# Kernel optimization log

Measured on AMD Instinct MI355X. Metric: run time of the kernel, lower is better.

The kernel has to match this reference:

```python
import jax, jax.numpy as jnp
import numpy as np

N = 10000
E = 320000
IN, HID, OUT = 512, 128, 128
HEADS, GC = 4, 64
NEG_SLOPE = 0.2


def setup_inputs() -> dict:
    key = jax.random.key(0)
    ks = jax.random.split(key, 12)
    inp = {
        'x': jax.random.normal(ks[0], (N, IN), dtype=jnp.float32),
        'edge_index': jax.random.randint(ks[1], (2, E), 0, N, dtype=jnp.int64),
        # encoder params
        'W1': jax.random.normal(ks[2], (IN, HID), dtype=jnp.float32) / np.sqrt(IN),
        'b1': jnp.zeros((HID,), dtype=jnp.float32),
        'W2': jax.random.normal(ks[3], (HID, OUT), dtype=jnp.float32) / np.sqrt(HID),
        'b2': jnp.zeros((OUT,), dtype=jnp.float32),
        # GATConv params: lin weight [OUT, HEADS*GC], att vectors [HEADS, GC], bias [HEADS*GC]
        'Wg': jax.random.normal(ks[4], (OUT, HEADS * GC), dtype=jnp.float32) / np.sqrt(OUT),
        'att_src': jax.random.normal(ks[5], (HEADS, GC), dtype=jnp.float32) * 0.1,
        'att_dst': jax.random.normal(ks[6], (HEADS, GC), dtype=jnp.float32) * 0.1,
        'bias_g': jnp.zeros((HEADS * GC,), dtype=jnp.float32),
    }
    return inp


def _forward(x, W1, b1, W2, b2, Wg, att_src, att_dst, bias_g, edge_index):
    # encoder: Linear -> ReLU -> Linear
    h = jax.nn.relu(x @ W1 + b1) @ W2 + b2  # [N, OUT]
    # GATConv adds self-loops by default
    loops = jnp.arange(N, dtype=edge_index.dtype)
    src = jnp.concatenate([edge_index[0], loops])  # message sources j
    dst = jnp.concatenate([edge_index[1], loops])  # message targets i
    # per-head linear transform
    g = (h @ Wg).reshape(N, HEADS, GC)  # [N, H, C]
    a_src = jnp.sum(g * att_src, axis=-1)  # [N, H]
    a_dst = jnp.sum(g * att_dst, axis=-1)  # [N, H]
    e = a_src[src] + a_dst[dst]            # [E+N, H]
    e = jax.nn.leaky_relu(e, NEG_SLOPE)
    # segment softmax over incoming edges of each destination node
    m = jax.ops.segment_max(e, dst, num_segments=N)  # [N, H]
    ex = jnp.exp(e - m[dst])
    s = jax.ops.segment_sum(ex, dst, num_segments=N)  # [N, H]
    alpha = ex / s[dst]                    # [E+N, H]
    # weighted scatter-aggregate of source features
    out = jax.ops.segment_sum(g[src] * alpha[:, :, None], dst, num_segments=N)  # [N, H, C]
    return out.reshape(N, HEADS * GC) + bias_g


def reference(x, edge_index, W1, b1, W2, b2, Wg, att_src, att_dst, bias_g):
    return _forward(x, W1, b1, W2, b2, Wg, att_src, att_dst, bias_g, edge_index)
```

## Files before the change

kernel.cpp:

```cpp
#include <hip/hip_runtime.h>

#define N_NODES 10000
#define N_EDGES 320000
#define DIM_IN  512
#define DIM_HID 128
#define HC      256
#define NEG_SLOPE 0.2f
#define SLOT    96

typedef short short8 __attribute__((ext_vector_type(8)));
typedef float floatx4 __attribute__((ext_vector_type(4)));

__device__ __forceinline__ unsigned short f2bf(float x) {
  unsigned int u = __float_as_uint(x);
  u += 0x7FFFu + ((u >> 16) & 1u);
  return (unsigned short)(u >> 16);
}

__global__ __launch_bounds__(256) void prep_kernel(
    const float* __restrict__ W2, const float* __restrict__ Wg,
    const float* __restrict__ b2, const float* __restrict__ W1,
    const float* __restrict__ x,
    unsigned short* __restrict__ WfT, float* __restrict__ bfuse,
    unsigned short* __restrict__ W1T, unsigned short* __restrict__ xb,
    int* __restrict__ cursor) {
  __shared__ float Ast[16][68];
  __shared__ float Bsf[16][64];
  __shared__ unsigned short td[32][33];
  const int t = threadIdx.x;
  const int b = blockIdx.x;
  if (b >= 76) {
    const int base = (b - 76) * 2048 + t * 8;
    const float4 v0 = *(const float4*)(x + base);
    const float4 v1 = *(const float4*)(x + base + 4);
    ushort4 s0 = {f2bf(v0.x), f2bf(v0.y), f2bf(v0.z), f2bf(v0.w)};
    ushort4 s1 = {f2bf(v1.x), f2bf(v1.y), f2bf(v1.z), f2bf(v1.w)};
    *(ushort4*)(xb + base)     = s0;
    *(ushort4*)(xb + base + 4) = s1;
    return;
  }
  if (b < 12) {
    const int flat = b * 256 + t;
    if (flat < (N_NODES + 3) / 4) ((int4*)cursor)[flat] = make_int4(0, 0, 0, 0);
    const int bx = b >> 2, by = b & 3;
    const int tx = t & 15, ty = t >> 4;
    const int m0 = bx * 64, n0 = by * 64;
    const int ar = t >> 2, ac4 = (t & 3) * 4;
    const int br = t >> 4, bc4 = (t & 15) * 4;
    const int arow = m0 + ar;
    float acc[4][4] = {};
    float4 av, bv, avn, bvn;
    auto gload = [&](int k0, float4& a4, float4& b4) {
      if (arow < DIM_HID)       a4 = *(const float4*)(W2 + (size_t)arow * DIM_HID + k0 + ac4);
      else if (arow == DIM_HID) a4 = *(const float4*)(b2 + k0 + ac4);
      else                      a4 = make_float4(0.f, 0.f, 0.f, 0.f);
      b4 = *(const float4*)(Wg + (size_t)(k0 + br) * HC + n0 + bc4);
    };
    gload(0, av, bv);
    for (int k0 = 0; k0 < DIM_HID; k0 += 16) {
      Ast[ac4 + 0][ar] = av.x; Ast[ac4 + 1][ar] = av.y;
      Ast[ac4 + 2][ar] = av.z; Ast[ac4 + 3][ar] = av.w;
      *(float4*)&Bsf[br][bc4] = bv;
      __syncthreads();
      if (k0 + 16 < DIM_HID) gload(k0 + 16, avn, bvn);
#pragma unroll
      for (int kk = 0; kk < 16; ++kk) {
        const float4 a = *(const float4*)&Ast[kk][ty * 4];
        const float4 bq = *(const float4*)&Bsf[kk][tx * 4];
        const float as[4] = {a.x, a.y, a.z, a.w};
        const float bs[4] = {bq.x, bq.y, bq.z, bq.w};
#pragma unroll
        for (int i = 0; i < 4; ++i)
#pragma unroll
          for (int j = 0; j < 4; ++j) acc[i][j] = fmaf(as[i], bs[j], acc[i][j]);
      }
      __syncthreads();
      av = avn; bv = bvn;
    }
#pragma unroll
    for (int i = 0; i < 4; ++i) {
      const int row = m0 + ty * 4 + i;
#pragma unroll
      for (int j = 0; j < 4; ++j) {
        const int col = n0 + tx * 4 + j;
        if (row < DIM_HID)       WfT[(size_t)col * DIM_HID + row] = f2bf(acc[i][j]);
        else if (row == DIM_HID) bfuse[col] = acc[i][j];
      }
    }
  } else {
    const int bb = b - 12;
    const int r0 = (bb >> 2) * 32, c0 = (bb & 3) * 32;
    const int tx = t & 31, ty = t >> 5;
#pragma unroll
    for (int p = 0; p < 4; ++p)
      td[tx][ty + p * 8] = f2bf(W1[(size_t)(r0 + ty + p * 8) * DIM_HID + c0 + tx]);
    __syncthreads();
#pragma unroll
    for (int p = 0; p < 4; ++p)
      W1T[(size_t)(c0 + ty + p * 8) * DIM_IN + r0 + tx] = td[ty + p * 8][tx];
  }
}

__global__ __launch_bounds__(256) void gemm1_kernel(
    const unsigned short* __restrict__ xb, const unsigned short* __restrict__ W1T,
    const float* __restrict__ b1, unsigned short* __restrict__ h1b) {
  constexpr int K = DIM_IN, N = DIM_HID, BK = 32;
  __shared__ unsigned short As[64][48];
  __shared__ unsigned short Bs[32][48];
  const int t = threadIdx.x;
  const int m0 = blockIdx.x * 64, n0 = blockIdx.y * 32;
  const int w = t >> 6, L = t & 63, lm = L & 15, q = L >> 4;
  floatx4 acc[2] = {};
  uint4 ab, abn;
  uint2 bb, bbn;
  auto ld = [&](int kb, uint4& va, uint2& vb) {
    va = *(const uint4*)(xb + (size_t)(m0 + (t >> 2)) * K + kb + (t & 3) * 8);
    vb = *(const uint2*)(W1T + (size_t)(n0 + (t >> 3)) * K + kb + (t & 7) * 4);
  };
  constexpr int NT = K / BK;
  ld(0, ab, bb);
  for (int kt = 0; kt < NT; ++kt) {
    *(uint4*)&As[t >> 2][(t & 3) * 8] = ab;
    *(uint2*)&Bs[t >> 3][(t & 7) * 4] = bb;
    __syncthreads();
    if (kt + 1 < NT) ld((kt + 1) * BK, abn, bbn);
    const short8 af = *(const short8*)&As[w * 16 + lm][q * 8];
#pragma unroll
    for (int nt = 0; nt < 2; ++nt) {
      const short8 bf = *(const short8*)&Bs[nt * 16 + lm][q * 8];
      acc[nt] = __builtin_amdgcn_mfma_f32_16x16x32_bf16(af, bf, acc[nt], 0, 0, 0);
    }
    __syncthreads();
    ab = abn; bb = bbn;
  }
  const int row0 = m0 + w * 16 + q * 4;
#pragma unroll
  for (int nt = 0; nt < 2; ++nt) {
    const int col = n0 + nt * 16 + lm;
    const float bv = b1[col];
#pragma unroll
    for (int r = 0; r < 4; ++r)
      if (row0 + r < N_NODES)
        h1b[(size_t)(row0 + r) * N + col] = f2bf(fmaxf(acc[nt][r] + bv, 0.f));
  }
}

__global__ __launch_bounds__(256) void gemm2_kernel(
    const unsigned short* __restrict__ h1b, const unsigned short* __restrict__ WfT,
    const float* __restrict__ bfuse, unsigned short* __restrict__ g,
    const float* __restrict__ att_src, const float* __restrict__ att_dst,
    float* __restrict__ a_src, float* __restrict__ a_dst,
    const int* __restrict__ e_src, const int* __restrict__ e_dst,
    int* __restrict__ cursor, int* __restrict__ src_sorted) {
  constexpr int K = DIM_HID, N = HC, BK = 32;
  __shared__ unsigned short As[64][48];
  __shared__ unsigned short Bs[64][48];
  const int t = threadIdx.x;
  {
    const int nthr = gridDim.x * gridDim.y * 256;
    const int flat = (blockIdx.y * gridDim.x + blockIdx.x) * 256 + t;
    for (int id = flat; id < N_EDGES + N_NODES; id += nthr) {
      int s, d;
      if (id < N_EDGES) { s = e_src[id]; d = e_dst[id]; }
      else              { s = d = id - N_EDGES; }
      src_sorted[d * SLOT + atomicAdd(&cursor[d], 1)] = s;
    }
  }
  const int m0 = blockIdx.x * 64, n0 = blockIdx.y * 64;
  const int w = t >> 6, L = t & 63, lm = L & 15, q = L >> 4;
  floatx4 acc[4] = {};
  uint4 ab, abn, bb, bbn;
  auto ld = [&](int kb, uint4& va, uint4& vb) {
    va = *(const uint4*)(h1b + (size_t)(m0 + (t >> 2)) * K + kb + (t & 3) * 8);
    vb = *(const uint4*)(WfT + (size_t)(n0 + (t >> 2)) * K + kb + (t & 3) * 8);
  };
  constexpr int NT = K / BK;
  ld(0, ab, bb);
  for (int kt = 0; kt < NT; ++kt) {
    *(uint4*)&As[t >> 2][(t & 3) * 8] = ab;
    *(uint4*)&Bs[t >> 2][(t & 3) * 8] = bb;
    __syncthreads();
    if (kt + 1 < NT) ld((kt + 1) * BK, abn, bbn);
    const short8 af = *(const short8*)&As[w * 16 + lm][q * 8];
#pragma unroll
    for (int nt = 0; nt < 4; ++nt) {
      const short8 bf = *(const short8*)&Bs[nt * 16 + lm][q * 8];
      acc[nt] = __builtin_amdgcn_mfma_f32_16x16x32_bf16(af, bf, acc[nt], 0, 0, 0);
    }
    __syncthreads();
    ab = abn; bb = bbn;
  }
  const int row0 = m0 + w * 16 + q * 4;
  const int hh = n0 >> 6;
  float ps[4] = {}, pd[4] = {};
#pragma unroll
  for (int nt = 0; nt < 4; ++nt) {
    const int col = n0 + nt * 16 + lm;
    const float bv = bfuse[col];
    const float as_c = att_src[hh * 64 + nt * 16 + lm];
    const float ad_c = att_dst[hh * 64 + nt * 16 + lm];
#pragma unroll
    for (int r = 0; r < 4; ++r) {
      const float gv = acc[nt][r] + bv;
      if (row0 + r < N_NODES) g[(size_t)(row0 + r) * N + col] = f2bf(gv);
      ps[r] = fmaf(gv, as_c, ps[r]);
      pd[r] = fmaf(gv, ad_c, pd[r]);
    }
  }
#pragma unroll
  for (int r = 0; r < 4; ++r) {
#pragma unroll
    for (int off = 1; off < 16; off <<= 1) {
      ps[r] += __shfl_xor(ps[r], off);
      pd[r] += __shfl_xor(pd[r], off);
    }
    if (lm == 0 && row0 + r < N_NODES) {
      a_src[(row0 + r) * 4 + hh] = ps[r];
      a_dst[(row0 + r) * 4 + hh] = pd[r];
    }
  }
}

__global__ __launch_bounds__(256) void aggregate_kernel(
    const unsigned short* __restrict__ g, const float* __restrict__ a_src,
    const float* __restrict__ a_dst, const int* __restrict__ cursor,
    const int* __restrict__ src_sorted, const float* __restrict__ bias_g,
    float* __restrict__ out) {
  const int wv   = threadIdx.x >> 6;
  const int lane = threadIdx.x & 63;
  const int node = blockIdx.x * 4 + wv;
  if (node >= N_NODES) return;
  const int e2 = lane >> 5;
  const int c8 = lane & 31;
  const int h  = c8 >> 3;
  const int start = node * SLOT;
  const int end   = start + cursor[node];
  const float4 ad = *(const float4*)(a_dst + node * 4);

  float a[8] = {};
  float s_loc = 0.f;
  for (int base = start; base < end; base += 64) {
    const int rem = min(64, end - base);
    int   sidxL = 0;
    float w0 = 0.f, w1 = 0.f, w2 = 0.f, w3 = 0.f;
    if (lane < rem) {
      sidxL = src_sorted[base + lane];
      const float4 as4 = *(const float4*)(a_src + sidxL * 4);
      float e0 = as4.x + ad.x; e0 = (e0 > 0.f) ? e0 : NEG_SLOPE * e0;
      float e1 = as4.y + ad.y; e1 = (e1 > 0.f) ? e1 : NEG_SLOPE * e1;
      float ee = as4.z + ad.z; ee = (ee > 0.f) ? ee : NEG_SLOPE * ee;
      float e3 = as4.w + ad.w; e3 = (e3 > 0.f) ? e3 : NEG_SLOPE * e3;
      w0 = __expf(e0); w1 = __expf(e1); w2 = __expf(ee); w3 = __expf(e3);
    }
    const int half = (rem + 1) >> 1;
#pragma unroll 4
    for (int k = 0; k < half; ++k) {
      const int j  = 2 * k + e2;
      const int js = (j < rem) ? j : (rem - 1);
      const int sj = __shfl(sidxL, js);
      const float f0 = __shfl(w0, js), f1 = __shfl(w1, js);
      const float f2 = __shfl(w2, js), f3 = __shfl(w3, js);
      float w = (h & 2) ? ((h & 1) ? f3 : f2) : ((h & 1) ? f1 : f0);
      if (j >= rem) w = 0.f;
      const uint4 gv = *(const uint4*)(g + (size_t)sj * HC + c8 * 8);
      s_loc += w;
      a[0] = fmaf(w, __uint_as_float(gv.x << 16), a[0]);
      a[1] = fmaf(w, __uint_as_float(gv.x & 0xFFFF0000u), a[1]);
      a[2] = fmaf(w, __uint_as_float(gv.y << 16), a[2]);
      a[3] = fmaf(w, __uint_as_float(gv.y & 0xFFFF0000u), a[3]);
      a[4] = fmaf(w, __uint_as_float(gv.z << 16), a[4]);
      a[5] = fmaf(w, __uint_as_float(gv.z & 0xFFFF0000u), a[5]);
      a[6] = fmaf(w, __uint_as_float(gv.w << 16), a[6]);
      a[7] = fmaf(w, __uint_as_float(gv.w & 0xFFFF0000u), a[7]);
    }
  }
#pragma unroll
  for (int k = 0; k < 8; ++k) a[k] += __shfl_xor(a[k], 32);
  s_loc += __shfl_xor(s_loc, 32);
  if (e2 == 0) {
    const float inv = 1.f / s_loc;
    const float4 b0 = *(const float4*)(bias_g + c8 * 8);
    const float4 b1v = *(const float4*)(bias_g + c8 * 8 + 4);
    float4 o0, o1;
    o0.x = a[0] * inv + b0.x;  o0.y = a[1] * inv + b0.y;
    o0.z = a[2] * inv + b0.z;  o0.w = a[3] * inv + b0.w;
    o1.x = a[4] * inv + b1v.x; o1.y = a[5] * inv + b1v.y;
    o1.z = a[6] * inv + b1v.z; o1.w = a[7] * inv + b1v.w;
    float* op = out + (size_t)node * HC + c8 * 8;
    *(float4*)op = o0;
    *(float4*)(op + 4) = o1;
  }
}

extern "C" void kernel_launch(void* const* d_in, const int* in_sizes, int n_in,
                              void* d_out, int out_size, void* d_ws, size_t ws_size,
                              hipStream_t stream) {
  const float* x       = (const float*)d_in[0];
  const int*   ei      = (const int*)d_in[1];
  const float* W1      = (const float*)d_in[2];
  const float* b1      = (const float*)d_in[3];
  const float* W2      = (const float*)d_in[4];
  const float* b2      = (const float*)d_in[5];
  const float* Wg      = (const float*)d_in[6];
  const float* att_src = (const float*)d_in[7];
  const float* att_dst = (const float*)d_in[8];
  const float* bias_g  = (const float*)d_in[9];
  float* out = (float*)d_out;

  char* ws = (char*)d_ws;
  unsigned short* xb  = (unsigned short*)ws; ws += (size_t)(N_NODES + 64) * DIM_IN * 2;
  unsigned short* h1b = (unsigned short*)ws; ws += (size_t)(N_NODES + 64) * DIM_HID * 2;
  unsigned short* g   = (unsigned short*)ws; ws += (size_t)N_NODES * HC * 2;
  unsigned short* W1T = (unsigned short*)ws; ws += (size_t)DIM_HID * DIM_IN * 2;
  unsigned short* WfT = (unsigned short*)ws; ws += (size_t)HC * DIM_HID * 2;
  float* bfuse   = (float*)ws; ws += (size_t)HC * 4;
  float* a_src   = (float*)ws; ws += (size_t)N_NODES * 4 * 4;
  float* a_dst   = (float*)ws; ws += (size_t)N_NODES * 4 * 4;
  int* cursor    = (int*)ws;   ws += (size_t)N_NODES * 4;
  int* src_sorted= (int*)ws;   ws += (size_t)N_NODES * SLOT * 4;

  const dim3 blk(256);
  prep_kernel<<<76 + 2500, blk, 0, stream>>>(
      W2, Wg, b2, W1, x, WfT, bfuse, W1T, xb, cursor);
  gemm1_kernel<<<dim3(157, 4), blk, 0, stream>>>(xb, W1T, b1, h1b);
  gemm2_kernel<<<dim3(157, 4), blk, 0, stream>>>(
      h1b, WfT, bfuse, g, att_src, att_dst, a_src, a_dst,
      ei, ei + N_EDGES, cursor, src_sorted);
  aggregate_kernel<<<(N_NODES + 3) / 4, blk, 0, stream>>>(
      g, a_src, a_dst, cursor, src_sorted, bias_g, out);
}
```

Before: 152.2 us.

## Fuse x bf16 conversion into gemm1 and retile both GEMMs to full-width tiles

Drops the separate pass that converts x to bf16 and instead loads fp32 x directly in gemm1, converting it while staging into shared memory. That removes one write and one re-read of a 10 MB intermediate. Both GEMMs now use 32-row tiles that span the full output width, so each block reads its A rows only once, at the cost of each block staging the whole weight matrix. gemm2 maps one wave to each head for the attention dot products, and the aggregate inner loop unroll is raised from 4 to 8. The grids are smaller, so fewer blocks share the edge-bucketing work.

```diff
diff --git a/kernel.cpp b/kernel.cpp
--- a/kernel.cpp
+++ b/kernel.cpp
@@ -20,25 +20,13 @@
 __global__ __launch_bounds__(256) void prep_kernel(
     const float* __restrict__ W2, const float* __restrict__ Wg,
     const float* __restrict__ b2, const float* __restrict__ W1,
-    const float* __restrict__ x,
     unsigned short* __restrict__ WfT, float* __restrict__ bfuse,
-    unsigned short* __restrict__ W1T, unsigned short* __restrict__ xb,
-    int* __restrict__ cursor) {
+    unsigned short* __restrict__ W1T, int* __restrict__ cursor) {
   __shared__ float Ast[16][68];
   __shared__ float Bsf[16][64];
   __shared__ unsigned short td[32][33];
   const int t = threadIdx.x;
   const int b = blockIdx.x;
-  if (b >= 76) {
-    const int base = (b - 76) * 2048 + t * 8;
-    const float4 v0 = *(const float4*)(x + base);
-    const float4 v1 = *(const float4*)(x + base + 4);
-    ushort4 s0 = {f2bf(v0.x), f2bf(v0.y), f2bf(v0.z), f2bf(v0.w)};
-    ushort4 s1 = {f2bf(v1.x), f2bf(v1.y), f2bf(v1.z), f2bf(v1.w)};
-    *(ushort4*)(xb + base)     = s0;
-    *(ushort4*)(xb + base + 4) = s1;
-    return;
-  }
   if (b < 12) {
     const int flat = b * 256 + t;
     if (flat < (N_NODES + 3) / 4) ((int4*)cursor)[flat] = make_int4(0, 0, 0, 0);
@@ -102,46 +90,58 @@
 }
 
 __global__ __launch_bounds__(256) void gemm1_kernel(
-    const unsigned short* __restrict__ xb, const unsigned short* __restrict__ W1T,
+    const float* __restrict__ x, const unsigned short* __restrict__ W1T,
     const float* __restrict__ b1, unsigned short* __restrict__ h1b) {
   constexpr int K = DIM_IN, N = DIM_HID, BK = 32;
-  __shared__ unsigned short As[64][48];
-  __shared__ unsigned short Bs[32][48];
+  __shared__ unsigned short As[32][40];
+  __shared__ unsigned short Bs[128][40];
   const int t = threadIdx.x;
-  const int m0 = blockIdx.x * 64, n0 = blockIdx.y * 32;
+  const int m0 = blockIdx.x * 32;
   const int w = t >> 6, L = t & 63, lm = L & 15, q = L >> 4;
-  floatx4 acc[2] = {};
-  uint4 ab, abn;
-  uint2 bb, bbn;
-  auto ld = [&](int kb, uint4& va, uint2& vb) {
-    va = *(const uint4*)(xb + (size_t)(m0 + (t >> 2)) * K + kb + (t & 3) * 8);
-    vb = *(const uint2*)(W1T + (size_t)(n0 + (t >> 3)) * K + kb + (t & 7) * 4);
+  floatx4 acc[2][2] = {};
+  const int arow = t >> 3, akoff = (t & 7) * 4;
+  const int bcol = t >> 1, bkoff = (t & 1) * 16;
+  float4 av, avn;
+  uint4 vb0, vb1, vb0n, vb1n;
+  auto ld = [&](int kb, float4& a4, uint4& b0, uint4& b1r) {
+    a4 = (m0 + arow < N_NODES)
+        ? *(const float4*)(x + (size_t)(m0 + arow) * K + kb + akoff)
+        : make_float4(0.f, 0.f, 0.f, 0.f);
+    b0  = *(const uint4*)(W1T + (size_t)bcol * K + kb + bkoff);
+    b1r = *(const uint4*)(W1T + (size_t)bcol * K + kb + bkoff + 8);
   };
   constexpr int NT = K / BK;
-  ld(0, ab, bb);
+  ld(0, av, vb0, vb1);
   for (int kt = 0; kt < NT; ++kt) {
-    *(uint4*)&As[t >> 2][(t & 3) * 8] = ab;
-    *(uint2*)&Bs[t >> 3][(t & 7) * 4] = bb;
-    __syncthreads();
-    if (kt + 1 < NT) ld((kt + 1) * BK, abn, bbn);
-    const short8 af = *(const short8*)&As[w * 16 + lm][q * 8];
+    ushort4 s0 = {f2bf(av.x), f2bf(av.y), f2bf(av.z), f2bf(av.w)};
+    *(ushort4*)&As[arow][akoff] = s0;
+    *(uint4*)&Bs[bcol][bkoff]     = vb0;
+    *(uint4*)&Bs[bcol][bkoff + 8] = vb1;
+    __syncthreads();
+    if (kt + 1 < NT) ld((kt + 1) * BK, avn, vb0n, vb1n);
+    const short8 af0 = *(const short8*)&As[lm][q * 8];
+    const short8 af1 = *(const short8*)&As[16 + lm][q * 8];
 #pragma unroll
     for (int nt = 0; nt < 2; ++nt) {
-      const short8 bf = *(const short8*)&Bs[nt * 16 + lm][q * 8];
-      acc[nt] = __builtin_amdgcn_mfma_f32_16x16x32_bf16(af, bf, acc[nt], 0, 0, 0);
-    }
-    __syncthreads();
-    ab = abn; bb = bbn;
-  }
-  const int row0 = m0 + w * 16 + q * 4;
-#pragma unroll
-  for (int nt = 0; nt < 2; ++nt) {
-    const int col = n0 + nt * 16 + lm;
-    const float bv = b1[col];
-#pragma unroll
-    for (int r = 0; r < 4; ++r)
-      if (row0 + r < N_NODES)
-        h1b[(size_t)(row0 + r) * N + col] = f2bf(fmaxf(acc[nt][r] + bv, 0.f));
+      const short8 bf = *(const short8*)&Bs[w * 32 + nt * 16 + lm][q * 8];
+      acc[0][nt] = __builtin_amdgcn_mfma_f32_16x16x32_bf16(af0, bf, acc[0][nt], 0, 0, 0);
+      acc[1][nt] = __builtin_amdgcn_mfma_f32_16x16x32_bf16(af1, bf, acc[1][nt], 0, 0, 0);
+    }
+    __syncthreads();
+    av = avn; vb0 = vb0n; vb1 = vb1n;
+  }
+#pragma unroll
+  for (int mt = 0; mt < 2; ++mt) {
+    const int row0 = m0 + mt * 16 + q * 4;
+#pragma unroll
+    for (int nt = 0; nt < 2; ++nt) {
+      const int col = w * 32 + nt * 16 + lm;
+      const float bv = b1[col];
+#pragma unroll
+      for (int r = 0; r < 4; ++r)
+        if (row0 + r < N_NODES)
+          h1b[(size_t)(row0 + r) * N + col] = f2bf(fmaxf(acc[mt][nt][r] + bv, 0.f));
+    }
   }
 }
 
@@ -153,12 +153,12 @@
     const int* __restrict__ e_src, const int* __restrict__ e_dst,
     int* __restrict__ cursor, int* __restrict__ src_sorted) {
   constexpr int K = DIM_HID, N = HC, BK = 32;
-  __shared__ unsigned short As[64][48];
-  __shared__ unsigned short Bs[64][48];
+  __shared__ unsigned short As[32][40];
+  __shared__ unsigned short Bs[256][40];
   const int t = threadIdx.x;
   {
-    const int nthr = gridDim.x * gridDim.y * 256;
-    const int flat = (blockIdx.y * gridDim.x + blockIdx.x) * 256 + t;
+    const int nthr = gridDim.x * 256;
+    const int flat = blockIdx.x * 256 + t;
     for (int id = flat; id < N_EDGES + N_NODES; id += nthr) {
       int s, d;
       if (id < N_EDGES) { s = e_src[id]; d = e_dst[id]; }
@@ -166,57 +166,72 @@
       src_sorted[d * SLOT + atomicAdd(&cursor[d], 1)] = s;
     }
   }
-  const int m0 = blockIdx.x * 64, n0 = blockIdx.y * 64;
+  const int m0 = blockIdx.x * 32;
   const int w = t >> 6, L = t & 63, lm = L & 15, q = L >> 4;
-  floatx4 acc[4] = {};
-  uint4 ab, abn, bb, bbn;
-  auto ld = [&](int kb, uint4& va, uint4& vb) {
-    va = *(const uint4*)(h1b + (size_t)(m0 + (t >> 2)) * K + kb + (t & 3) * 8);
-    vb = *(const uint4*)(WfT + (size_t)(n0 + (t >> 2)) * K + kb + (t & 3) * 8);
+  floatx4 acc[2][4] = {};
+  const int arow = t >> 3, akoff = (t & 7) * 4;
+  uint2 va, van;
+  uint4 vb[4], vbn[4];
+  auto ld = [&](int kb, uint2& a2, uint4* b4) {
+    a2 = *(const uint2*)(h1b + (size_t)(m0 + arow) * K + kb + akoff);
+#pragma unroll
+    for (int j = 0; j < 4; ++j)
+      b4[j] = *(const uint4*)(WfT + (size_t)t * K + kb + j * 8);
   };
   constexpr int NT = K / BK;
-  ld(0, ab, bb);
+  ld(0, va, vb);
   for (int kt = 0; kt < NT; ++kt) {
-    *(uint4*)&As[t >> 2][(t & 3) * 8] = ab;
-    *(uint4*)&Bs[t >> 2][(t & 3) * 8] = bb;
-    __syncthreads();
-    if (kt + 1 < NT) ld((kt + 1) * BK, abn, bbn);
-    const short8 af = *(const short8*)&As[w * 16 + lm][q * 8];
+    *(uint2*)&As[arow][akoff] = va;
+#pragma unroll
+    for (int j = 0; j < 4; ++j) *(uint4*)&Bs[t][j * 8] = vb[j];
+    __syncthreads();
+    if (kt + 1 < NT) ld((kt + 1) * BK, van, vbn);
+    const short8 af0 = *(const short8*)&As[lm][q * 8];
+    const short8 af1 = *(const short8*)&As[16 + lm][q * 8];
 #pragma unroll
     for (int nt = 0; nt < 4; ++nt) {
-      const short8 bf = *(const short8*)&Bs[nt * 16 + lm][q * 8];
-      acc[nt] = __builtin_amdgcn_mfma_f32_16x16x32_bf16(af, bf, acc[nt], 0, 0, 0);
-    }
-    __syncthreads();
-    ab = abn; bb = bbn;
-  }
-  const int row0 = m0 + w * 16 + q * 4;
-  const int hh = n0 >> 6;
-  float ps[4] = {}, pd[4] = {};
+      const short8 bf = *(const short8*)&Bs[w * 64 + nt * 16 + lm][q * 8];
+      acc[0][nt] = __builtin_amdgcn_mfma_f32_16x16x32_bf16(af0, bf, acc[0][nt], 0, 0, 0);
+      acc[1][nt] = __builtin_amdgcn_mfma_f32_16x16x32_bf16(af1, bf, acc[1][nt], 0, 0, 0);
+    }
+    __syncthreads();
+    va = van;
+#pragma unroll
+    for (int j = 0; j < 4; ++j) vb[j] = vbn[j];
+  }
+  float ps[2][4] = {}, pd[2][4] = {};
 #pragma unroll
   for (int nt = 0; nt < 4; ++nt) {
-    const int col = n0 + nt * 16 + lm;
+    const int col = w * 64 + nt * 16 + lm;
     const float bv = bfuse[col];
-    const float as_c = att_src[hh * 64 + nt * 16 + lm];
-    const float ad_c = att_dst[hh * 64 + nt * 16 + lm];
+    const float as_c = att_src[col];
+    const float ad_c = att_dst[col];
+#pragma unroll
+    for (int mt = 0; mt < 2; ++mt) {
+      const int row0 = m0 + mt * 16 + q * 4;
+#pragma unroll
+      for (int r = 0; r < 4; ++r) {
+        const float gv = acc[mt][nt][r] + bv;
+        if (row0 + r < N_NODES) g[(size_t)(row0 + r) * N + col] = f2bf(gv);
+        ps[mt][r] = fmaf(gv, as_c, ps[mt][r]);
+        pd[mt][r] = fmaf(gv, ad_c, pd[mt][r]);
+      }
+    }
+  }
+#pragma unroll
+  for (int mt = 0; mt < 2; ++mt) {
+    const int row0 = m0 + mt * 16 + q * 4;
 #pragma unroll
     for (int r = 0; r < 4; ++r) {
-      const float gv = acc[nt][r] + bv;
-      if (row0 + r < N_NODES) g[(size_t)(row0 + r) * N + col] = f2bf(gv);
-      ps[r] = fmaf(gv, as_c, ps[r]);
-      pd[r] = fmaf(gv, ad_c, pd[r]);
-    }
-  }
-#pragma unroll
-  for (int r = 0; r < 4; ++r) {
-#pragma unroll
-    for (int off = 1; off < 16; off <<= 1) {
-      ps[r] += __shfl_xor(ps[r], off);
-      pd[r] += __shfl_xor(pd[r], off);
-    }
-    if (lm == 0 && row0 + r < N_NODES) {
-      a_src[(row0 + r) * 4 + hh] = ps[r];
-      a_dst[(row0 + r) * 4 + hh] = pd[r];
+#pragma unroll
+      for (int off = 1; off < 16; off <<= 1) {
+        ps[mt][r] += __shfl_xor(ps[mt][r], off);
+        pd[mt][r] += __shfl_xor(pd[mt][r], off);
+      }
+      if (lm == 0 && row0 + r < N_NODES) {
+        a_src[(row0 + r) * 4 + w] = ps[mt][r];
+        a_dst[(row0 + r) * 4 + w] = pd[mt][r];
+      }
     }
   }
 }
@@ -253,7 +268,7 @@
       w0 = __expf(e0); w1 = __expf(e1); w2 = __expf(ee); w3 = __expf(e3);
     }
     const int half = (rem + 1) >> 1;
-#pragma unroll 4
+#pragma unroll 8
     for (int k = 0; k < half; ++k) {
       const int j  = 2 * k + e2;
       const int js = (j < rem) ? j : (rem - 1);
@@ -308,7 +323,6 @@
   float* out = (float*)d_out;
 
   char* ws = (char*)d_ws;
-  unsigned short* xb  = (unsigned short*)ws; ws += (size_t)(N_NODES + 64) * DIM_IN * 2;
   unsigned short* h1b = (unsigned short*)ws; ws += (size_t)(N_NODES + 64) * DIM_HID * 2;
   unsigned short* g   = (unsigned short*)ws; ws += (size_t)N_NODES * HC * 2;
   unsigned short* W1T = (unsigned short*)ws; ws += (size_t)DIM_HID * DIM_IN * 2;
@@ -320,10 +334,9 @@
   int* src_sorted= (int*)ws;   ws += (size_t)N_NODES * SLOT * 4;
 
   const dim3 blk(256);
-  prep_kernel<<<76 + 2500, blk, 0, stream>>>(
-      W2, Wg, b2, W1, x, WfT, bfuse, W1T, xb, cursor);
-  gemm1_kernel<<<dim3(157, 4), blk, 0, stream>>>(xb, W1T, b1, h1b);
-  gemm2_kernel<<<dim3(157, 4), blk, 0, stream>>>(
+  prep_kernel<<<76, blk, 0, stream>>>(W2, Wg, b2, W1, WfT, bfuse, W1T, cursor);
+  gemm1_kernel<<<313, blk, 0, stream>>>(x, W1T, b1, h1b);
+  gemm2_kernel<<<313, blk, 0, stream>>>(
       h1b, WfT, bfuse, g, att_src, att_dst, a_src, a_dst,
       ei, ei + N_EDGES, cursor, src_sorted);
   aggregate_kernel<<<(N_NODES + 3) / 4, blk, 0, stream>>>(
```

Measured after the change: 167.4 us. 10.0% more time.

## Fuse x/W1 bf16 conversion into first GEMM and merge prep with it

Applied to the files above, without the earlier changes.

Removes the separate prep pass that converted x to bf16 and transposed W1. The first GEMM now loads fp32 x and W1 directly, converts them to bf16 in registers and transposes W1 into shared memory. The W2·Wg fusion and cursor zeroing run as extra blocks in the same launch. This saves one kernel launch and the round trip of the bf16 copy of x through global memory. In exchange, each of the four column blocks re-reads fp32 x at twice the bytes, and shared-memory stores for the transposed W1 tile may hit bank conflicts.

```diff
diff --git a/kernel.cpp b/kernel.cpp
--- a/kernel.cpp
+++ b/kernel.cpp
@@ -17,131 +17,122 @@
   return (unsigned short)(u >> 16);
 }
 
-__global__ __launch_bounds__(256) void prep_kernel(
+union Sm1 {
+  struct { unsigned short As[64][48]; unsigned short Bs[32][48]; } g;
+  struct { float Ast[16][68]; float Bsf[16][64]; } p;
+};
+
+__global__ __launch_bounds__(256) void fused1_kernel(
+    const float* __restrict__ x, const float* __restrict__ W1,
+    const float* __restrict__ b1,
     const float* __restrict__ W2, const float* __restrict__ Wg,
-    const float* __restrict__ b2, const float* __restrict__ W1,
-    const float* __restrict__ x,
-    unsigned short* __restrict__ WfT, float* __restrict__ bfuse,
-    unsigned short* __restrict__ W1T, unsigned short* __restrict__ xb,
-    int* __restrict__ cursor) {
-  __shared__ float Ast[16][68];
-  __shared__ float Bsf[16][64];
-  __shared__ unsigned short td[32][33];
+    const float* __restrict__ b2,
+    unsigned short* __restrict__ h1b, unsigned short* __restrict__ WfT,
+    float* __restrict__ bfuse, int* __restrict__ cursor) {
+  __shared__ Sm1 sm;
   const int t = threadIdx.x;
   const int b = blockIdx.x;
-  if (b >= 76) {
-    const int base = (b - 76) * 2048 + t * 8;
-    const float4 v0 = *(const float4*)(x + base);
-    const float4 v1 = *(const float4*)(x + base + 4);
-    ushort4 s0 = {f2bf(v0.x), f2bf(v0.y), f2bf(v0.z), f2bf(v0.w)};
-    ushort4 s1 = {f2bf(v1.x), f2bf(v1.y), f2bf(v1.z), f2bf(v1.w)};
-    *(ushort4*)(xb + base)     = s0;
-    *(ushort4*)(xb + base + 4) = s1;
-    return;
-  }
-  if (b < 12) {
-    const int flat = b * 256 + t;
-    if (flat < (N_NODES + 3) / 4) ((int4*)cursor)[flat] = make_int4(0, 0, 0, 0);
-    const int bx = b >> 2, by = b & 3;
-    const int tx = t & 15, ty = t >> 4;
-    const int m0 = bx * 64, n0 = by * 64;
-    const int ar = t >> 2, ac4 = (t & 3) * 4;
-    const int br = t >> 4, bc4 = (t & 15) * 4;
-    const int arow = m0 + ar;
-    float acc[4][4] = {};
-    float4 av, bv, avn, bvn;
-    auto gload = [&](int k0, float4& a4, float4& b4) {
-      if (arow < DIM_HID)       a4 = *(const float4*)(W2 + (size_t)arow * DIM_HID + k0 + ac4);
-      else if (arow == DIM_HID) a4 = *(const float4*)(b2 + k0 + ac4);
-      else                      a4 = make_float4(0.f, 0.f, 0.f, 0.f);
-      b4 = *(const float4*)(Wg + (size_t)(k0 + br) * HC + n0 + bc4);
+
+  if (b < 628) {
+    constexpr int K = DIM_IN, N = DIM_HID, BK = 32;
+    const int m0 = (b % 157) * 64, n0 = (b / 157) * 32;
+    const int w = t >> 6, L = t & 63, lm = L & 15, q = L >> 4;
+    floatx4 acc[2] = {};
+    const int ar = t >> 3, ac = (t & 7) * 4;
+    float4 va0, va1, vb, va0n, va1n, vbn;
+    auto ld = [&](int kb, float4& a0, float4& a1, float4& bw) {
+      a0 = (m0 + ar < N_NODES)
+          ? *(const float4*)(x + (size_t)(m0 + ar) * K + kb + ac)
+          : make_float4(0.f, 0.f, 0.f, 0.f);
+      a1 = (m0 + ar + 32 < N_NODES)
+          ? *(const float4*)(x + (size_t)(m0 + ar + 32) * K + kb + ac)
+          : make_float4(0.f, 0.f, 0.f, 0.f);
+      bw = *(const float4*)(W1 + (size_t)(kb + ar) * N + n0 + ac);
     };
-    gload(0, av, bv);
-    for (int k0 = 0; k0 < DIM_HID; k0 += 16) {
-      Ast[ac4 + 0][ar] = av.x; Ast[ac4 + 1][ar] = av.y;
-      Ast[ac4 + 2][ar] = av.z; Ast[ac4 + 3][ar] = av.w;
-      *(float4*)&Bsf[br][bc4] = bv;
+    constexpr int NT = K / BK;
+    ld(0, va0, va1, vb);
+    for (int kt = 0; kt < NT; ++kt) {
+      ushort4 s0 = {f2bf(va0.x), f2bf(va0.y), f2bf(va0.z), f2bf(va0.w)};
+      ushort4 s1 = {f2bf(va1.x), f2bf(va1.y), f2bf(va1.z), f2bf(va1.w)};
+      *(ushort4*)&sm.g.As[ar][ac]      = s0;
+      *(ushort4*)&sm.g.As[ar + 32][ac] = s1;
+      sm.g.Bs[ac + 0][ar] = f2bf(vb.x);
+      sm.g.Bs[ac + 1][ar] = f2bf(vb.y);
+      sm.g.Bs[ac + 2][ar] = f2bf(vb.z);
+      sm.g.Bs[ac + 3][ar] = f2bf(vb.w);
       __syncthreads();
-      if (k0 + 16 < DIM_HID) gload(k0 + 16, avn, bvn);
-#pragma unroll
-      for (int kk = 0; kk < 16; ++kk) {
-        const float4 a = *(const float4*)&Ast[kk][ty * 4];
-        const float4 bq = *(const float4*)&Bsf[kk][tx * 4];
-        const float as[4] = {a.x, a.y, a.z, a.w};
-        const float bs[4] = {bq.x, bq.y, bq.z, bq.w};
-#pragma unroll
-        for (int i = 0; i < 4; ++i)
-#pragma unroll
-          for (int j = 0; j < 4; ++j) acc[i][j] = fmaf(as[i], bs[j], acc[i][j]);
+      if (kt + 1 < NT) ld((kt + 1) * BK, va0n, va1n, vbn);
+      const short8 af = *(const short8*)&sm.g.As[w * 16 + lm][q * 8];
+#pragma unroll
+      for (int nt = 0; nt < 2; ++nt) {
+        const short8 bf = *(const short8*)&sm.g.Bs[nt * 16 + lm][q * 8];
+        acc[nt] = __builtin_amdgcn_mfma_f32_16x16x32_bf16(af, bf, acc[nt], 0, 0, 0);
       }
       __syncthreads();
-      av = avn; bv = bvn;
-    }
-#pragma unroll
-    for (int i = 0; i < 4; ++i) {
-      const int row = m0 + ty * 4 + i;
-#pragma unroll
-      for (int j = 0; j < 4; ++j) {
-        const int col = n0 + tx * 4 + j;
-        if (row < DIM_HID)       WfT[(size_t)col * DIM_HID + row] = f2bf(acc[i][j]);
-        else if (row == DIM_HID) bfuse[col] = acc[i][j];
-      }
-    }
-  } else {
-    const int bb = b - 12;
-    const int r0 = (bb >> 2) * 32, c0 = (bb & 3) * 32;
-    const int tx = t & 31, ty = t >> 5;
-#pragma unroll
-    for (int p = 0; p < 4; ++p)
-      td[tx][ty + p * 8] = f2bf(W1[(size_t)(r0 + ty + p * 8) * DIM_HID + c0 + tx]);
+      va0 = va0n; va1 = va1n; vb = vbn;
+    }
+    const int row0 = m0 + w * 16 + q * 4;
+#pragma unroll
+    for (int nt = 0; nt < 2; ++nt) {
+      const int col = n0 + nt * 16 + lm;
+      const float bv = b1[col];
+#pragma unroll
+      for (int r = 0; r < 4; ++r)
+        if (row0 + r < N_NODES)
+          h1b[(size_t)(row0 + r) * N + col] = f2bf(fmaxf(acc[nt][r] + bv, 0.f));
+    }
+    return;
+  }
+
+  const int bp = b - 628;
+  {
+    const int flat = bp * 256 + t;
+    if (flat < (N_NODES + 3) / 4) ((int4*)cursor)[flat] = make_int4(0, 0, 0, 0);
+  }
+  const int bx = bp >> 2, by = bp & 3;
+  const int tx = t & 15, ty = t >> 4;
+  const int m0 = bx * 64, n0 = by * 64;
+  const int ar = t >> 2, ac4 = (t & 3) * 4;
+  const int br = t >> 4, bc4 = (t & 15) * 4;
+  const int arow = m0 + ar;
+  float acc[4][4] = {};
+  float4 av, bv, avn, bvn;
+  auto gload = [&](int k0, float4& a4, float4& b4) {
+    if (arow < DIM_HID)       a4 = *(const float4*)(W2 + (size_t)arow * DIM_HID + k0 + ac4);
+    else if (arow == DIM_HID) a4 = *(const float4*)(b2 + k0 + ac4);
+    else                      a4 = make_float4(0.f, 0.f, 0.f, 0.f);
+    b4 = *(const float4*)(Wg + (size_t)(k0 + br) * HC + n0 + bc4);
+  };
+  gload(0, av, bv);
+  for (int k0 = 0; k0 < DIM_HID; k0 += 16) {
+    sm.p.Ast[ac4 + 0][ar] = av.x; sm.p.Ast[ac4 + 1][ar] = av.y;
+    sm.p.Ast[ac4 + 2][ar] = av.z; sm.p.Ast[ac4 + 3][ar] = av.w;
+    *(float4*)&sm.p.Bsf[br][bc4] = bv;
     __syncthreads();
-#pragma unroll
-    for (int p = 0; p < 4; ++p)
-      W1T[(size_t)(c0 + ty + p * 8) * DIM_IN + r0 + tx] = td[ty + p * 8][tx];
-  }
-}
-
-__global__ __launch_bounds__(256) void gemm1_kernel(
-    const unsigned short* __restrict__ xb, const unsigned short* __restrict__ W1T,
-    const float* __restrict__ b1, unsigned short* __restrict__ h1b) {
-  constexpr int K = DIM_IN, N = DIM_HID, BK = 32;
-  __shared__ unsigned short As[64][48];
-  __shared__ unsigned short Bs[32][48];
-  const int t = threadIdx.x;
-  const int m0 = blockIdx.x * 64, n0 = blockIdx.y * 32;
-  const int w = t >> 6, L = t & 63, lm = L & 15, q = L >> 4;
-  floatx4 acc[2] = {};
-  uint4 ab, abn;
-  uint2 bb, bbn;
-  auto ld = [&](int kb, uint4& va, uint2& vb) {
-    va = *(const uint4*)(xb + (size_t)(m0 + (t >> 2)) * K + kb + (t & 3) * 8);
-    vb = *(const uint2*)(W1T + (size_t)(n0 + (t >> 3)) * K + kb + (t & 7) * 4);
-  };
-  constexpr int NT = K / BK;
-  ld(0, ab, bb);
-  for (int kt = 0; kt < NT; ++kt) {
-    *(uint4*)&As[t >> 2][(t & 3) * 8] = ab;
-    *(uint2*)&Bs[t >> 3][(t & 7) * 4] = bb;
+    if (k0 + 16 < DIM_HID) gload(k0 + 16, avn, bvn);
+#pragma unroll
+    for (int kk = 0; kk < 16; ++kk) {
+      const float4 a = *(const float4*)&sm.p.Ast[kk][ty * 4];
+      const float4 bq = *(const float4*)&sm.p.Bsf[kk][tx * 4];
+      const float as[4] = {a.x, a.y, a.z, a.w};
+      const float bs[4] = {bq.x, bq.y, bq.z, bq.w};
+#pragma unroll
+      for (int i = 0; i < 4; ++i)
+#pragma unroll
+        for (int j = 0; j < 4; ++j) acc[i][j] = fmaf(as[i], bs[j], acc[i][j]);
+    }
     __syncthreads();
-    if (kt + 1 < NT) ld((kt + 1) * BK, abn, bbn);
-    const short8 af = *(const short8*)&As[w * 16 + lm][q * 8];
-#pragma unroll
-    for (int nt = 0; nt < 2; ++nt) {
-      const short8 bf = *(const short8*)&Bs[nt * 16 + lm][q * 8];
-      acc[nt] = __builtin_amdgcn_mfma_f32_16x16x32_bf16(af, bf, acc[nt], 0, 0, 0);
-    }
-    __syncthreads();
-    ab = abn; bb = bbn;
-  }
-  const int row0 = m0 + w * 16 + q * 4;
-#pragma unroll
-  for (int nt = 0; nt < 2; ++nt) {
-    const int col = n0 + nt * 16 + lm;
-    const float bv = b1[col];
-#pragma unroll
-    for (int r = 0; r < 4; ++r)
-      if (row0 + r < N_NODES)
-        h1b[(size_t)(row0 + r) * N + col] = f2bf(fmaxf(acc[nt][r] + bv, 0.f));
+    av = avn; bv = bvn;
+  }
+#pragma unroll
+  for (int i = 0; i < 4; ++i) {
+    const int row = m0 + ty * 4 + i;
+#pragma unroll
+    for (int j = 0; j < 4; ++j) {
+      const int col = n0 + tx * 4 + j;
+      if (row < DIM_HID)       WfT[(size_t)col * DIM_HID + row] = f2bf(acc[i][j]);
+      else if (row == DIM_HID) bfuse[col] = acc[i][j];
+    }
   }
 }
 
@@ -308,10 +299,8 @@
   float* out = (float*)d_out;
 
   char* ws = (char*)d_ws;
-  unsigned short* xb  = (unsigned short*)ws; ws += (size_t)(N_NODES + 64) * DIM_IN * 2;
   unsigned short* h1b = (unsigned short*)ws; ws += (size_t)(N_NODES + 64) * DIM_HID * 2;
   unsigned short* g   = (unsigned short*)ws; ws += (size_t)N_NODES * HC * 2;
-  unsigned short* W1T = (unsigned short*)ws; ws += (size_t)DIM_HID * DIM_IN * 2;
   unsigned short* WfT = (unsigned short*)ws; ws += (size_t)HC * DIM_HID * 2;
   float* bfuse   = (float*)ws; ws += (size_t)HC * 4;
   float* a_src   = (float*)ws; ws += (size_t)N_NODES * 4 * 4;
@@ -320,9 +309,8 @@
   int* src_sorted= (int*)ws;   ws += (size_t)N_NODES * SLOT * 4;
 
   const dim3 blk(256);
-  prep_kernel<<<76 + 2500, blk, 0, stream>>>(
-      W2, Wg, b2, W1, x, WfT, bfuse, W1T, xb, cursor);
-  gemm1_kernel<<<dim3(157, 4), blk, 0, stream>>>(xb, W1T, b1, h1b);
+  fused1_kernel<<<640, blk, 0, stream>>>(
+      x, W1, b1, W2, Wg, b2, h1b, WfT, bfuse, cursor);
   gemm2_kernel<<<dim3(157, 4), blk, 0, stream>>>(
       h1b, WfT, bfuse, g, att_src, att_dst, a_src, a_dst,
       ei, ei + N_EDGES, cursor, src_sorted);
```

Measured after the change: 151.7 us. No clear change (-0.3%).
